# Optimization experiments

Hardware: AMD Instinct MI355X
Metric: run time of the kernel (lower is better)

Reference implementation:

```python
import jax, jax.numpy as jnp
import numpy as np
import math

D = 768; H = 12; DH = 64; LAT = 512; B = 2; L = 1024


def _rms(x, w, eps=1e-6):
    return w * x * jax.lax.rsqrt(jnp.mean(x * x, axis=-1, keepdims=True) + eps)


def _rope_tables(seq_len, dh):
    inv = 1.0 / (10000.0 ** (np.arange(0, dh, 2, dtype=np.float32) / dh))
    t = np.arange(seq_len, dtype=np.float32)
    f = np.outer(t, inv)
    emb = np.concatenate([f, f], axis=-1)
    return jnp.asarray(np.cos(emb))[None, :, None, :], jnp.asarray(np.sin(emb))[None, :, None, :]


def _rope(x, cos, sin):
    x1, x2 = jnp.split(x, 2, axis=-1)
    return x * cos + jnp.concatenate([-x2, x1], axis=-1) * sin


def setup_inputs():
    key = jax.random.key(0)
    ks = jax.random.split(key, 8)
    s = 0.02
    return {
        'x': jax.random.normal(ks[0], (B, L, D), jnp.float32),
        'w_ln': jnp.ones((D,), jnp.float32),
        'w_compress': jax.random.normal(ks[1], (D, LAT), jnp.float32) * s,
        'w_qkv': jax.random.normal(ks[2], (LAT, 3 * D), jnp.float32) * s,
        'w_reso': jax.random.normal(ks[3], (LAT, H * 4), jnp.float32) * s,
        'w_qn': jnp.ones((DH,), jnp.float32),
        'w_kn': jnp.ones((DH,), jnp.float32),
        'head_decay': jnp.linspace(-3.0, 1.0, H).astype(jnp.float32),
        'temperature': jnp.ones((1,), jnp.float32) * 0.5,
        'w_out_gate': jax.random.normal(ks[4], (LAT, D), jnp.float32) * s,
        'w_proj': jax.random.normal(ks[5], (D, D), jnp.float32) * s,
        'w_memnorm': jnp.ones((D,), jnp.float32),
    }


def reference(x, w_ln, w_compress, w_qkv, w_reso, w_qn, w_kn, head_decay, temperature, w_out_gate, w_proj, w_memnorm):
    cos, sin = _rope_tables(L, DH)
    xn = _rms(x, w_ln)
    latent = jax.nn.silu(xn @ w_compress)                        # (B,L,LAT)
    q, k, v = jnp.split(latent @ w_qkv, 3, axis=-1)
    q = _rope(_rms(q.reshape(B, L, H, DH), w_qn), cos, sin)
    k = _rope(_rms(k.reshape(B, L, H, DH), w_kn), cos, sin)
    v_f = v.reshape(B, L, H, DH)
    q_f = jax.nn.elu(q) + 1.0
    k_f = jax.nn.elu(k) + 1.0
    params = (latent @ w_reso).reshape(B, L, H, 4)
    sem_amp, sem_phase, ctx_amp, ctx_phase = [params[..., i] for i in range(4)]
    sem_phase = jax.nn.sigmoid(sem_phase) * math.pi
    ctx_phase = jax.nn.sigmoid(ctx_phase) * math.pi
    decay = jnp.clip(0.3 + 0.65 * jax.nn.sigmoid(head_decay), 1e-5, 0.999)   # (H,)
    gate = jnp.clip(jax.nn.sigmoid(jax.nn.sigmoid(sem_amp) * jax.nn.sigmoid(ctx_amp)
                                   * jnp.cos(sem_phase - ctx_phase) * temperature[0]) * 1.2 - 0.1,
                    0.05, 0.95)                                  # (B,L,H)
    one_m = (1.0 - decay)[None, None, :]                          # (1,1,H)
    kv_in = jnp.einsum('blhd,blhe->blhde', k_f, v_f) * gate[..., None, None] * one_m[..., None, None]
    z_in = k_f * one_m[..., None]
    # cumulative log-decay -> df, same as torch cumsum of constant per-step log_decay
    cum_log = jnp.arange(1, L + 1, dtype=jnp.float32)[:, None] * jnp.log(decay)[None, :]
    df = jnp.exp(cum_log)[None, :, :, None]                       # (1,L,H,1)
    kv_states = jnp.cumsum(kv_in / (df[..., None] + 1e-8), axis=1) * df[..., None]
    z_states = jnp.cumsum(z_in / (df + 1e-8), axis=1) * df
    out_num = jnp.einsum('blhd,blhde->blhe', q_f, kv_states)
    den = jnp.clip(jnp.sum(q_f * z_states, axis=-1, keepdims=True), 1e-5, None)
    out = (out_num / den).reshape(B, L, D)
    return (_rms(out, w_memnorm) @ w_proj) * jax.nn.silu(latent @ w_out_gate)
```

## Files before the change

kernel.cpp:

```cpp
#include <hip/hip_runtime.h>
#include <hip/hip_bf16.h>
#include <math.h>

#define D_MODEL 768
#define NHEAD   12
#define LATD    512
#define BATCH   2
#define SEQ     1024
#define NROWS   (BATCH*SEQ)
#define NCHUNK  (SEQ/64)
#define NBH     (BATCH*NHEAD)
#define NFUSE   3200
#define PQ      72

using short8 = __attribute__((ext_vector_type(8))) short;
using f32x4  = __attribute__((ext_vector_type(4))) float;

__device__ __forceinline__ float sigf(float x){ return 1.f/(1.f+expf(-x)); }
__device__ __forceinline__ float decay_of(float hd){
  float d = 0.3f + 0.65f*sigf(hd);
  return fminf(fmaxf(d, 1e-5f), 0.999f);
}
__device__ __forceinline__ unsigned short f2b(float f){
  __hip_bfloat16 h = __float2bfloat16(f);
  return *reinterpret_cast<unsigned short*>(&h);
}
__device__ __forceinline__ float bf2f(unsigned short u){
  unsigned int x = ((unsigned int)u) << 16;
  return __uint_as_float(x);
}
__device__ __forceinline__ void async16(const unsigned short* g, unsigned short* l){
  __builtin_amdgcn_global_load_lds((const __attribute__((address_space(1))) void*)g,
                                   (__attribute__((address_space(3))) void*)l, 16, 0, 0);
}

__device__ __forceinline__ void rms_row(const float* __restrict__ xr,
    const float* __restrict__ w, unsigned short* __restrict__ yr,
    int tid, float* red)
{
  float v0 = xr[tid], v1 = xr[tid+256], v2 = xr[tid+512];
  float s = v0*v0 + v1*v1 + v2*v2;
  #pragma unroll
  for (int off=32; off; off>>=1) s += __shfl_xor(s, off, 64);
  if ((tid & 63) == 0) red[tid>>6] = s;
  __syncthreads();
  s = red[0]+red[1]+red[2]+red[3];
  float sc = rsqrtf(s*(1.f/(float)D_MODEL) + 1e-6f);
  yr[tid]     = f2b(v0*sc*w[tid]);
  yr[tid+256] = f2b(v1*sc*w[tid+256]);
  yr[tid+512] = f2b(v2*sc*w[tid+512]);
}

__global__ __launch_bounds__(256) void k_rmsnorm_bf(const float* __restrict__ x,
    const float* __restrict__ w, unsigned short* __restrict__ y)
{
  __shared__ float red[4];
  int row = blockIdx.x, tid = threadIdx.x;
  rms_row(x + (size_t)row*D_MODEL, w, y + (size_t)row*D_MODEL, tid, red);
}

__global__ __launch_bounds__(256) void k_prep(
    const float* __restrict__ x, const float* __restrict__ w_ln,
    unsigned short* __restrict__ xn,
    const float* __restrict__ wc, const float* __restrict__ wq,
    const float* __restrict__ wr, const float* __restrict__ wg,
    const float* __restrict__ wp,
    unsigned short* __restrict__ wtc, unsigned short* __restrict__ wtq,
    unsigned short* __restrict__ wtg, unsigned short* __restrict__ wtp)
{
  __shared__ unsigned short tile[64][65];
  __shared__ float red[4];
  int blk = blockIdx.x, t = threadIdx.x;
  if (blk >= 640){
    int row = blk - 640;
    rms_row(x + (size_t)row*D_MODEL, w_ln, xn + (size_t)row*D_MODEL, t, red);
    return;
  }
  const float* W; unsigned short* WT; int K, N, bx, by;
  if (blk < 96){ W=wc; WT=wtc; K=768; N=512; bx=blk&7; by=blk>>3; }
  else if (blk < 384){ int i=blk-96;  W=wq; WT=wtq; K=512; N=2304; bx=i%36; by=i/36; }
  else if (blk < 480){ int i=blk-384; W=wg; WT=wtg; K=512; N=768;  bx=i%12; by=i/12; }
  else if (blk < 624){ int i=blk-480; W=wp; WT=wtp; K=768; N=768;  bx=i%12; by=i/12; }
  else {
    int i = blk - 624;
    #pragma unroll
    for (int j=0;j<16;j++){
      int e = i*4096 + t + j*256;
      int n = 2304 + (e >> 9), k = e & 511;
      float v = (n < 2352) ? wr[(size_t)k*48 + (n-2304)] : 0.f;
      wtq[(size_t)n*512 + k] = f2b(v);
    }
    return;
  }
  int k0 = by*64, n0 = bx*64, cr = t >> 6, cc = t & 63;
  #pragma unroll
  for (int i=0;i<16;i++){
    int r = cr + i*4;
    tile[r][cc] = f2b(W[(size_t)(k0+r)*N + n0 + cc]);
  }
  __syncthreads();
  #pragma unroll
  for (int i=0;i<16;i++){
    int nn = cr + i*4;
    WT[(size_t)(n0+nn)*K + k0 + cc] = tile[cc][nn];
  }
}

__global__ __launch_bounds__(256) void k_gemm64(const unsigned short* __restrict__ A,
    const unsigned short* __restrict__ BT, float* __restrict__ Cf,
    unsigned short* __restrict__ Cb, const unsigned short* __restrict__ auxb,
    int M, int N, int K, int act)
{
  __shared__ unsigned short As[64*64];
  __shared__ unsigned short Bs[64*64];
  int tid = threadIdx.x;
  int w = tid >> 6, lane = tid & 63;
  int m16 = lane & 15, quad = lane >> 4;
  int bm = blockIdx.y*64, bn = blockIdx.x*64;

  f32x4 acc[4];
  #pragma unroll
  for (int nt=0;nt<4;nt++) acc[nt] = (f32x4){0.f,0.f,0.f,0.f};

  for (int kk = 0; kk < K; kk += 64){
    #pragma unroll
    for (int i=0;i<2;i++){
      int g = (w*2 + i)*64 + lane;
      int m = g >> 3, c = (g & 7) ^ (m & 7);
      async16(A  + (size_t)(bm+m)*K + kk + c*8, As + (w*2+i)*512);
      async16(BT + (size_t)(bn+m)*K + kk + c*8, Bs + (w*2+i)*512);
    }
    __syncthreads();
    #pragma unroll
    for (int s=0;s<2;s++){
      int row = w*16 + m16;
      short8 af = *(const short8*)(As + (row*8 + ((s*4 + quad) ^ (row & 7)))*8);
      #pragma unroll
      for (int nt=0;nt<4;nt++){
        int n = nt*16 + m16;
        short8 bf = *(const short8*)(Bs + (n*8 + ((s*4 + quad) ^ (n & 7)))*8);
        acc[nt] = __builtin_amdgcn_mfma_f32_16x16x32_bf16(af, bf, acc[nt], 0, 0, 0);
      }
    }
    __syncthreads();
  }
  #pragma unroll
  for (int r=0;r<4;r++){
    int row = bm + w*16 + quad*4 + r;
    #pragma unroll
    for (int nt=0;nt<4;nt++){
      int col = bn + nt*16 + m16;
      float v = acc[nt][r];
      if (act == 1) v = v/(1.f + __expf(-v));
      else if (act == 2) v *= bf2f(auxb[(size_t)row*N + col]);
      if (Cf) Cf[(size_t)row*N + col] = v;
      if (Cb) Cb[(size_t)row*N + col] = f2b(v);
    }
  }
}

__global__ __launch_bounds__(256) void k_gemm_fused(const unsigned short* __restrict__ A,
    const unsigned short* __restrict__ BT, const float* __restrict__ w_qn,
    const float* __restrict__ w_kn, const float* __restrict__ hdec,
    const float* __restrict__ temp, unsigned short* __restrict__ qf,
    unsigned short* __restrict__ kf, unsigned short* __restrict__ vf,
    float* __restrict__ cKV, float* __restrict__ cG,
    unsigned short* __restrict__ gateb)
{
  __shared__ __align__(16) unsigned short SM[2*128*64];
  unsigned short* As = SM;
  unsigned short* Bs = SM + 128*64;
  const int K = LATD;
  int tid = threadIdx.x;
  int w = tid >> 6, lane = tid & 63;
  int wm = (w >> 1)*64, wn = (w & 1)*64;
  int m16 = lane & 15, quad = lane >> 4;
  int bm = blockIdx.y*128, bn = blockIdx.x*128;

  f32x4 acc[4][4];
  #pragma unroll
  for (int i=0;i<4;i++)
    #pragma unroll
    for (int j=0;j<4;j++) acc[i][j] = (f32x4){0.f,0.f,0.f,0.f};

  for (int kk = 0; kk < K; kk += 64){
    #pragma unroll
    for (int i=0;i<4;i++){
      int g = (w*4 + i)*64 + lane;
      int m = g >> 3, c = (g & 7) ^ (m & 7);
      async16(A  + (size_t)(bm+m)*K + kk + c*8, As + (w*4+i)*512);
      async16(BT + (size_t)(bn+m)*K + kk + c*8, Bs + (w*4+i)*512);
    }
    __syncthreads();
    #pragma unroll
    for (int s=0;s<2;s++){
      short8 af[4], bf[4];
      #pragma unroll
      for (int mt=0;mt<4;mt++){
        int m = wm + mt*16 + m16;
        int idx = m*8 + ((s*4 + quad) ^ (m & 7));
        af[mt] = *(const short8*)(As + idx*8);
      }
      #pragma unroll
      for (int nt=0;nt<4;nt++){
        int n = wn + nt*16 + m16;
        int idx = n*8 + ((s*4 + quad) ^ (n & 7));
        bf[nt] = *(const short8*)(Bs + idx*8);
      }
      #pragma unroll
      for (int mt=0;mt<4;mt++)
        #pragma unroll
        for (int nt=0;nt<4;nt++)
          acc[mt][nt] = __builtin_amdgcn_mfma_f32_16x16x32_bf16(af[mt], bf[nt], acc[mt][nt], 0, 0, 0);
    }
    __syncthreads();
  }

  int colbase = bn + wn;
  if (colbase < 2304){
    int sec = colbase >= 1536 ? 2 : (colbase >= 768 ? 1 : 0);
    int h = (colbase - sec*768) >> 6;
    if (sec == 2){
      #pragma unroll
      for (int mt=0;mt<4;mt++)
        #pragma unroll
        for (int r=0;r<4;r++){
          int row = bm + wm + mt*16 + quad*4 + r;
          int b = row >> 10, t = row & 1023;
          size_t ob = (((size_t)(b*NHEAD+h))*SEQ + t)*64;
          #pragma unroll
          for (int nt=0;nt<4;nt++)
            vf[ob + nt*16 + m16] = f2b(acc[mt][nt][r]);
        }
    } else {
      const float* wnp = sec ? w_kn : w_qn;
      unsigned short* of = sec ? kf : qf;
      float wv4[4];
      #pragma unroll
      for (int nt=0;nt<4;nt++) wv4[nt] = wnp[nt*16 + m16];
      float inv0 = exp2f(-(float)m16*(1.f/32.f)*13.28771237954945f);
      float inv1 = inv0 * 0.01f;
      #pragma unroll
      for (int mt=0;mt<4;mt++)
        #pragma unroll
        for (int r=0;r<4;r++){
          int row = bm + wm + mt*16 + quad*4 + r;
          int b = row >> 10, t = row & 1023;
          float s = 0.f;
          #pragma unroll
          for (int nt=0;nt<4;nt++) s += acc[mt][nt][r]*acc[mt][nt][r];
          s += __shfl_xor(s, 1, 64); s += __shfl_xor(s, 2, 64);
          s += __shfl_xor(s, 4, 64); s += __shfl_xor(s, 8, 64);
          float rs = rsqrtf(s*(1.f/64.f) + 1e-6f);
          float qv[4];
          #pragma unroll
          for (int nt=0;nt<4;nt++) qv[nt] = acc[mt][nt][r]*rs*wv4[nt];
          float s0,c0,s1,c1;
          __sincosf((float)t*inv0, &s0, &c0);
          __sincosf((float)t*inv1, &s1, &c1);
          size_t ob = (((size_t)(b*NHEAD+h))*SEQ + t)*64;
          #pragma unroll
          for (int nt=0;nt<4;nt++){
            float rot = (nt < 2) ? -qv[nt+2] : qv[nt-2];
            float cs = (nt & 1) ? c1 : c0, sn = (nt & 1) ? s1 : s0;
            float val = qv[nt]*cs + rot*sn;
            val = (val > 0.f) ? val + 1.f : __expf(val);
            of[ob + nt*16 + m16] = f2b(val);
          }
        }
    }
  } else if (colbase < 2432){
    float* pf = (float*)SM;
    if (colbase == 2304){
      #pragma unroll
      for (int mt=0;mt<4;mt++)
        #pragma unroll
        for (int r=0;r<4;r++){
          int rowl = wm + mt*16 + quad*4 + r;
          #pragma unroll
          for (int nt=0;nt<4;nt++){
            int p = nt*16 + m16;
            if (p < 48) pf[rowl*49 + p] = acc[mt][nt][r];
          }
        }
    }
    __syncthreads();
    float tv = temp[0];
    #pragma unroll
    for (int i=0;i<6;i++){
      int idx2 = tid + i*256;
      int rowl = idx2 / 12, h = idx2 - rowl*12;
      int row = bm + rowl, b = row >> 10, t = row & 1023;
      const float* pr = pf + rowl*49 + h*4;
      float sa = sigf(pr[0]);
      float sp = sigf(pr[1])*3.14159265358979323846f;
      float ca = sigf(pr[2]);
      float cp = sigf(pr[3])*3.14159265358979323846f;
      float z = sa*ca*cosf(sp - cp)*tv;
      float gate = fminf(fmaxf(sigf(z)*1.2f - 0.1f, 0.05f), 0.95f);
      float dd = decay_of(hdec[h]);
      float df = expf((float)(t+1)*logf(dd));
      float g = df/(df + 1e-8f);
      int ci = (b*NHEAD + h)*SEQ + t;
      cKV[ci] = g*gate*(1.f - dd);
      cG[ci]  = 1.f/gate;
    }
  } else {
    #pragma unroll
    for (int mt=0;mt<4;mt++)
      #pragma unroll
      for (int r=0;r<4;r++){
        int row = bm + wm + mt*16 + quad*4 + r;
        #pragma unroll
        for (int nt=0;nt<4;nt++){
          int gc = colbase + nt*16 + m16 - 2432;
          float v = acc[mt][nt][r];
          v = v/(1.f + __expf(-v));
          gateb[(size_t)row*D_MODEL + gc] = f2b(v);
        }
      }
  }
}

__global__ __launch_bounds__(256) void k_intra(const unsigned short* __restrict__ qf,
    const unsigned short* __restrict__ kf, const unsigned short* __restrict__ vf,
    const float* __restrict__ cKVb, const float* __restrict__ cGb,
    const float* __restrict__ hdec, float* __restrict__ numb,
    float* __restrict__ denb, float* __restrict__ Pb, float* __restrict__ zPb)
{
  __shared__ __align__(16) unsigned short Qb[64*PQ];
  __shared__ __align__(16) unsigned short Kb[64*PQ];
  __shared__ __align__(16) unsigned short KtS[64*PQ];
  __shared__ __align__(16) unsigned short Wb[64*PQ];
  __shared__ __align__(16) unsigned short Vt[80*PQ];
  __shared__ float cn[64], cps[64];
  int bid = blockIdx.x;
  int chunk = bid & 15, bh = bid >> 4, h = bh % NHEAD;
  int tid = threadIdx.x, w = tid >> 6, lane = tid & 63;
  int m16 = lane & 15, quad = lane >> 4;
  size_t base = ((size_t)bh*SEQ + chunk*64)*64;
  float d = decay_of(hdec[h]);
  float l2d = log2f(d);

  if (tid < 64){
    float c = cKVb[bh*SEQ + chunk*64 + tid];
    float pw = exp2f((float)(63 - tid)*l2d);
    cn[tid] = c;
    cps[tid] = c*pw;
    Vt[64*PQ + tid] = f2b(cGb[bh*SEQ + chunk*64 + tid]);
  }
  for (int i = tid; i < 15*PQ; i += 256) Vt[65*PQ + i] = 0;
  __syncthreads();

  #pragma unroll
  for (int i=0;i<2;i++){
    int g = tid + i*256;
    int r = g >> 3, c8 = (g & 7)*8;
    *(short8*)(Qb + r*PQ + c8) = *(const short8*)(qf + base + r*64 + c8);
    *(short8*)(Kb + r*PQ + c8) = *(const short8*)(kf + base + r*64 + c8);
  }
  {
    int s = tid & 63;
    float cpss = cps[s];
    #pragma unroll
    for (int i=0;i<2;i++){
      int c8 = ((tid >> 6) + i*4)*8;
      short8 vv = *(const short8*)(vf + base + s*64 + c8);
      short8 kk = *(const short8*)(kf + base + s*64 + c8);
      #pragma unroll
      for (int j=0;j<8;j++){
        Vt[(c8+j)*PQ + s] = ((unsigned short*)&vv)[j];
        KtS[(c8+j)*PQ + s] = f2b(bf2f(((unsigned short*)&kk)[j])*cpss);
      }
    }
  }
  __syncthreads();

  int trow = w*16 + quad*4;
  for (int stile=0; stile<4; stile++){
    if (stile > w){
      #pragma unroll
      for (int r=0;r<4;r++) Wb[(trow+r)*PQ + stile*16 + m16] = 0;
      continue;
    }
    f32x4 acc = (f32x4){0.f,0.f,0.f,0.f};
    #pragma unroll
    for (int ks=0;ks<2;ks++){
      short8 a = *(const short8*)(Qb + (w*16 + m16)*PQ + ks*32 + quad*8);
      short8 b = *(const short8*)(Kb + (stile*16 + m16)*PQ + ks*32 + quad*8);
      acc = __builtin_amdgcn_mfma_f32_16x16x32_bf16(a, b, acc, 0, 0, 0);
    }
    int s = stile*16 + m16;
    float cns = cn[s];
    #pragma unroll
    for (int r=0;r<4;r++){
      int t = trow + r;
      float wv = 0.f;
      if (s <= t) wv = acc[r]*exp2f((float)(t-s)*l2d)*cns;
      Wb[t*PQ + s] = f2b(wv);
    }
  }
  __syncthreads();

  {
    f32x4 acc[5];
    #pragma unroll
    for (int et=0;et<5;et++) acc[et] = (f32x4){0.f,0.f,0.f,0.f};
    #pragma unroll
    for (int et=0;et<5;et++)
      #pragma unroll
      for (int ks=0;ks<2;ks++){
        short8 a = *(const short8*)(Wb + (w*16 + m16)*PQ + ks*32 + quad*8);
        short8 b = *(const short8*)(Vt + (et*16 + m16)*PQ + ks*32 + quad*8);
        acc[et] = __builtin_amdgcn_mfma_f32_16x16x32_bf16(a, b, acc[et], 0, 0, 0);
      }
    #pragma unroll
    for (int et=0;et<4;et++)
      #pragma unroll
      for (int r=0;r<4;r++)
        numb[base + (size_t)(trow+r)*64 + et*16 + m16] = acc[et][r];
    if (m16 == 0){
      #pragma unroll
      for (int r=0;r<4;r++)
        denb[bh*SEQ + chunk*64 + trow + r] = acc[4][r];
    }
  }
  {
    #pragma unroll
    for (int j=0;j<5;j++){
      int tIdx = w + 4*j;
      int et = tIdx >> 2, dt = tIdx & 3;
      f32x4 acc = (f32x4){0.f,0.f,0.f,0.f};
      #pragma unroll
      for (int ks=0;ks<2;ks++){
        short8 a = *(const short8*)(Vt  + (et*16 + m16)*PQ + ks*32 + quad*8);
        short8 b = *(const short8*)(KtS + (dt*16 + m16)*PQ + ks*32 + quad*8);
        acc = __builtin_amdgcn_mfma_f32_16x16x32_bf16(a, b, acc, 0, 0, 0);
      }
      if (et < 4){
        #pragma unroll
        for (int r=0;r<4;r++)
          Pb[(size_t)bid*4096 + (et*16 + quad*4 + r)*64 + dt*16 + m16] = acc[r];
      } else {
        if (quad == 0) zPb[bid*64 + dt*16 + m16] = acc[0];
      }
    }
  }
}

__global__ __launch_bounds__(256) void k_scan(const float* __restrict__ Pb,
    const float* __restrict__ zPb, unsigned short* __restrict__ Sprev,
    unsigned short* __restrict__ zprev, const float* __restrict__ hdec)
{
  int bh = blockIdx.x >> 2, part = blockIdx.x & 3;
  int h = bh % NHEAD, tid = threadIdx.x;
  float d = decay_of(hdec[h]);
  float d64 = exp2f(64.f*log2f(d));
  int idx = part*1024 + tid*4;
  float4 S = make_float4(0.f,0.f,0.f,0.f);
  for (int c=0;c<NCHUNK;c++){
    size_t off = ((size_t)bh*NCHUNK + c)*4096 + idx;
    unsigned int lo = (unsigned int)f2b(S.x) | ((unsigned int)f2b(S.y) << 16);
    unsigned int hi = (unsigned int)f2b(S.z) | ((unsigned int)f2b(S.w) << 16);
    *(uint2*)(Sprev + off) = make_uint2(lo, hi);
    float4 p = *(const float4*)(Pb + off);
    S.x = S.x*d64 + p.x; S.y = S.y*d64 + p.y;
    S.z = S.z*d64 + p.z; S.w = S.w*d64 + p.w;
  }
  if (part == 0 && tid < 64){
    float z = 0.f;
    for (int c=0;c<NCHUNK;c++){
      int zoff = (bh*NCHUNK + c)*64 + tid;
      zprev[zoff] = f2b(z);
      z = z*d64 + zPb[zoff];
    }
  }
}

__global__ __launch_bounds__(256) void k_cross(const unsigned short* __restrict__ qf,
    const unsigned short* __restrict__ Sprev, const unsigned short* __restrict__ zprev,
    const float* __restrict__ numb, const float* __restrict__ denb,
    const float* __restrict__ hdec, float* __restrict__ attn)
{
  __shared__ __align__(16) unsigned short Qb[64*PQ];
  __shared__ __align__(16) unsigned short Sp[80*PQ];
  __shared__ float den_sm[64];
  int bid = blockIdx.x;
  int chunk = bid & 15, bh = bid >> 4, h = bh % NHEAD, b = bh / NHEAD;
  int tid = threadIdx.x, w = tid >> 6, lane = tid & 63;
  int m16 = lane & 15, quad = lane >> 4;
  size_t base = ((size_t)bh*SEQ + chunk*64)*64;
  float d = decay_of(hdec[h]);
  float l2d = log2f(d);

  #pragma unroll
  for (int i=0;i<2;i++){
    int g = tid + i*256;
    int r = g >> 3, c8 = (g & 7)*8;
    *(short8*)(Qb + r*PQ + c8) = *(const short8*)(qf + base + r*64 + c8);
    *(short8*)(Sp + r*PQ + c8) = *(const short8*)(Sprev + (size_t)bid*4096 + r*64 + c8);
  }
  if (tid < 64) Sp[64*PQ + tid] = zprev[bid*64 + tid];
  for (int i = tid; i < 15*PQ; i += 256) Sp[65*PQ + i] = 0;
  __syncthreads();

  f32x4 acc[5];
  #pragma unroll
  for (int et=0;et<5;et++) acc[et] = (f32x4){0.f,0.f,0.f,0.f};
  #pragma unroll
  for (int et=0;et<5;et++)
    #pragma unroll
    for (int ks=0;ks<2;ks++){
      short8 a = *(const short8*)(Qb + (w*16 + m16)*PQ + ks*32 + quad*8);
      short8 b = *(const short8*)(Sp + (et*16 + m16)*PQ + ks*32 + quad*8);
      acc[et] = __builtin_amdgcn_mfma_f32_16x16x32_bf16(a, b, acc[et], 0, 0, 0);
    }
  int trow = w*16 + quad*4;
  if (m16 == 0){
    #pragma unroll
    for (int r=0;r<4;r++){
      int tl = trow + r;
      float pw = exp2f((float)(tl+1)*l2d);
      float den = fmaxf(denb[bh*SEQ + chunk*64 + tl] + pw*acc[4][r], 1e-5f);
      den_sm[tl] = 1.f/den;
    }
  }
  __syncthreads();
  #pragma unroll
  for (int r=0;r<4;r++){
    int tl = trow + r;
    float pw = exp2f((float)(tl+1)*l2d);
    float invden = den_sm[tl];
    int tg = chunk*64 + tl;
    #pragma unroll
    for (int et=0;et<4;et++){
      int e = et*16 + m16;
      float nm = numb[base + (size_t)tl*64 + e] + pw*acc[et][r];
      attn[((size_t)(b*SEQ + tg))*D_MODEL + h*64 + e] = nm*invden;
    }
  }
}

extern "C" void kernel_launch(void* const* d_in, const int* in_sizes, int n_in,
                              void* d_out, int out_size, void* d_ws, size_t ws_size,
                              hipStream_t stream)
{
  (void)in_sizes; (void)n_in; (void)out_size; (void)ws_size;
  const float* x       = (const float*)d_in[0];
  const float* w_ln    = (const float*)d_in[1];
  const float* w_comp  = (const float*)d_in[2];
  const float* w_qkv   = (const float*)d_in[3];
  const float* w_reso  = (const float*)d_in[4];
  const float* w_qn    = (const float*)d_in[5];
  const float* w_kn    = (const float*)d_in[6];
  const float* hdec    = (const float*)d_in[7];
  const float* temp    = (const float*)d_in[8];
  const float* w_ogate = (const float*)d_in[9];
  const float* w_proj  = (const float*)d_in[10];
  const float* w_mn    = (const float*)d_in[11];
  float* ws = (float*)d_ws;
  float* out = (float*)d_out;

  const size_t o_cKV    = 0;
  const size_t o_cG     = o_cKV    + (size_t)NBH*SEQ;
  const size_t o_den    = o_cG     + (size_t)NBH*SEQ;
  const size_t o_P      = o_den    + (size_t)NBH*SEQ;
  const size_t o_zP     = o_P      + (size_t)NBH*NCHUNK*4096;
  const size_t o_attn   = o_zP     + (size_t)NBH*NCHUNK*64;
  const size_t o_numb   = o_attn   + (size_t)NROWS*D_MODEL;
  const size_t o_end    = o_numb   + (size_t)NBH*SEQ*64;

  unsigned short* bws = (unsigned short*)(ws + o_end);
  const size_t u_xn     = 0;
  const size_t u_latent = u_xn     + (size_t)NROWS*D_MODEL;
  const size_t u_memn   = u_latent + (size_t)NROWS*LATD;
  const size_t u_q      = u_memn   + (size_t)NROWS*D_MODEL;
  const size_t u_k      = u_q      + (size_t)NBH*SEQ*64;
  const size_t u_v      = u_k      + (size_t)NBH*SEQ*64;
  const size_t u_gate   = u_v      + (size_t)NBH*SEQ*64;
  const size_t u_S      = u_gate   + (size_t)NROWS*D_MODEL;
  const size_t u_zprev  = u_S      + (size_t)NBH*NCHUNK*4096;
  const size_t u_wtc    = u_zprev  + (size_t)NBH*NCHUNK*64;
  const size_t u_wtq    = u_wtc    + (size_t)LATD*D_MODEL;
  const size_t u_wtg    = u_wtq    + (size_t)2432*LATD;
  const size_t u_wtp    = u_wtg    + (size_t)D_MODEL*LATD;

  k_prep<<<2688, 256, 0, stream>>>(x, w_ln, bws + u_xn,
      w_comp, w_qkv, w_reso, w_ogate, w_proj,
      bws + u_wtc, bws + u_wtq, bws + u_wtg, bws + u_wtp);
  k_gemm64<<<dim3(LATD/64, NROWS/64), 256, 0, stream>>>(bws + u_xn, bws + u_wtc,
      nullptr, bws + u_latent, nullptr, NROWS, LATD, D_MODEL, 1);
  k_gemm_fused<<<dim3(NFUSE/128, NROWS/128), 256, 0, stream>>>(bws + u_latent, bws + u_wtq,
      w_qn, w_kn, hdec, temp, bws + u_q, bws + u_k, bws + u_v,
      ws + o_cKV, ws + o_cG, bws + u_gate);
  k_intra<<<NBH*NCHUNK, 256, 0, stream>>>(bws + u_q, bws + u_k, bws + u_v,
      ws + o_cKV, ws + o_cG, hdec, ws + o_numb, ws + o_den, ws + o_P, ws + o_zP);
  k_scan<<<NBH*4, 256, 0, stream>>>(ws + o_P, ws + o_zP, bws + u_S, bws + u_zprev, hdec);
  k_cross<<<NBH*NCHUNK, 256, 0, stream>>>(bws + u_q, bws + u_S, bws + u_zprev,
      ws + o_numb, ws + o_den, hdec, ws + o_attn);
  k_rmsnorm_bf<<<NROWS, 256, 0, stream>>>(ws + o_attn, w_mn, bws + u_memn);
  k_gemm64<<<dim3(D_MODEL/64, NROWS/64), 256, 0, stream>>>(bws + u_memn, bws + u_wtp,
      out, nullptr, bws + u_gate, NROWS, D_MODEL, D_MODEL, 2);
}
```

Measured before the change: 156.5 us.

## Fold chunk-state scan into cross kernel and swizzle block order for XCD locality

Removes the separate sequential scan kernel. Each cross block now rebuilds its prefix state directly as a decay-weighted sum over all earlier chunk contributions, which drops one launch and the Sprev/zprev round-trip through memory. In exchange, work grows quadratically with chunk index and Pb is re-read many times. Separately, the GEMM and cross kernels switch to a 1D grid with a mod-8 block swizzle, meant to group neighbouring tiles on the same XCD for better L2 reuse.

```diff
diff --git a/kernel.cpp b/kernel.cpp
--- a/kernel.cpp
+++ b/kernel.cpp
@@ -109,14 +109,17 @@
 __global__ __launch_bounds__(256) void k_gemm64(const unsigned short* __restrict__ A,
     const unsigned short* __restrict__ BT, float* __restrict__ Cf,
     unsigned short* __restrict__ Cb, const unsigned short* __restrict__ auxb,
-    int M, int N, int K, int act)
+    int M, int N, int K, int act, int NX)
 {
   __shared__ unsigned short As[64*64];
   __shared__ unsigned short Bs[64*64];
   int tid = threadIdx.x;
   int w = tid >> 6, lane = tid & 63;
   int m16 = lane & 15, quad = lane >> 4;
-  int bm = blockIdx.y*64, bn = blockIdx.x*64;
+  int bid = blockIdx.x, cpx = gridDim.x >> 3;
+  int swz = (bid & 7)*cpx + (bid >> 3);
+  int bx = swz % NX, by = swz / NX;
+  int bm = by*64, bn = bx*64;
 
   f32x4 acc[4];
   #pragma unroll
@@ -175,7 +178,10 @@
   int w = tid >> 6, lane = tid & 63;
   int wm = (w >> 1)*64, wn = (w & 1)*64;
   int m16 = lane & 15, quad = lane >> 4;
-  int bm = blockIdx.y*128, bn = blockIdx.x*128;
+  int bid = blockIdx.x;
+  int swz = (bid & 7)*50 + (bid >> 3);
+  int bx = swz >> 4, by = swz & 15;
+  int bm = by*128, bn = bx*128;
 
   f32x4 acc[4][4];
   #pragma unroll
@@ -448,37 +454,8 @@
   }
 }
 
-__global__ __launch_bounds__(256) void k_scan(const float* __restrict__ Pb,
-    const float* __restrict__ zPb, unsigned short* __restrict__ Sprev,
-    unsigned short* __restrict__ zprev, const float* __restrict__ hdec)
-{
-  int bh = blockIdx.x >> 2, part = blockIdx.x & 3;
-  int h = bh % NHEAD, tid = threadIdx.x;
-  float d = decay_of(hdec[h]);
-  float d64 = exp2f(64.f*log2f(d));
-  int idx = part*1024 + tid*4;
-  float4 S = make_float4(0.f,0.f,0.f,0.f);
-  for (int c=0;c<NCHUNK;c++){
-    size_t off = ((size_t)bh*NCHUNK + c)*4096 + idx;
-    unsigned int lo = (unsigned int)f2b(S.x) | ((unsigned int)f2b(S.y) << 16);
-    unsigned int hi = (unsigned int)f2b(S.z) | ((unsigned int)f2b(S.w) << 16);
-    *(uint2*)(Sprev + off) = make_uint2(lo, hi);
-    float4 p = *(const float4*)(Pb + off);
-    S.x = S.x*d64 + p.x; S.y = S.y*d64 + p.y;
-    S.z = S.z*d64 + p.z; S.w = S.w*d64 + p.w;
-  }
-  if (part == 0 && tid < 64){
-    float z = 0.f;
-    for (int c=0;c<NCHUNK;c++){
-      int zoff = (bh*NCHUNK + c)*64 + tid;
-      zprev[zoff] = f2b(z);
-      z = z*d64 + zPb[zoff];
-    }
-  }
-}
-
 __global__ __launch_bounds__(256) void k_cross(const unsigned short* __restrict__ qf,
-    const unsigned short* __restrict__ Sprev, const unsigned short* __restrict__ zprev,
+    const float* __restrict__ Pb, const float* __restrict__ zPb,
     const float* __restrict__ numb, const float* __restrict__ denb,
     const float* __restrict__ hdec, float* __restrict__ attn)
 {
@@ -486,21 +463,52 @@
   __shared__ __align__(16) unsigned short Sp[80*PQ];
   __shared__ float den_sm[64];
   int bid = blockIdx.x;
-  int chunk = bid & 15, bh = bid >> 4, h = bh % NHEAD, b = bh / NHEAD;
+  int swz = (bid & 7)*48 + (bid >> 3);
+  int chunk = swz & 15, bh = swz >> 4;
+  int h = bh % NHEAD, b = bh / NHEAD;
   int tid = threadIdx.x, w = tid >> 6, lane = tid & 63;
   int m16 = lane & 15, quad = lane >> 4;
   size_t base = ((size_t)bh*SEQ + chunk*64)*64;
   float d = decay_of(hdec[h]);
   float l2d = log2f(d);
+  float d64l2 = 64.f*l2d;
 
   #pragma unroll
   for (int i=0;i<2;i++){
     int g = tid + i*256;
     int r = g >> 3, c8 = (g & 7)*8;
     *(short8*)(Qb + r*PQ + c8) = *(const short8*)(qf + base + r*64 + c8);
-    *(short8*)(Sp + r*PQ + c8) = *(const short8*)(Sprev + (size_t)bid*4096 + r*64 + c8);
-  }
-  if (tid < 64) Sp[64*PQ + tid] = zprev[bid*64 + tid];
+  }
+
+  {
+    int r = tid >> 3, c8 = (tid & 7)*8;
+    float a0[8], a1[8];
+    #pragma unroll
+    for (int j=0;j<8;j++){ a0[j]=0.f; a1[j]=0.f; }
+    for (int c=0;c<chunk;c++){
+      float wgt = exp2f((float)(chunk-1-c)*d64l2);
+      const float* ps = Pb + ((size_t)(bh*NCHUNK + c))*4096;
+      float4 p0 = *(const float4*)(ps + r*64 + c8);
+      float4 p1 = *(const float4*)(ps + r*64 + c8 + 4);
+      float4 p2 = *(const float4*)(ps + (r+32)*64 + c8);
+      float4 p3 = *(const float4*)(ps + (r+32)*64 + c8 + 4);
+      a0[0]+=wgt*p0.x; a0[1]+=wgt*p0.y; a0[2]+=wgt*p0.z; a0[3]+=wgt*p0.w;
+      a0[4]+=wgt*p1.x; a0[5]+=wgt*p1.y; a0[6]+=wgt*p1.z; a0[7]+=wgt*p1.w;
+      a1[0]+=wgt*p2.x; a1[1]+=wgt*p2.y; a1[2]+=wgt*p2.z; a1[3]+=wgt*p2.w;
+      a1[4]+=wgt*p3.x; a1[5]+=wgt*p3.y; a1[6]+=wgt*p3.z; a1[7]+=wgt*p3.w;
+    }
+    #pragma unroll
+    for (int j=0;j<8;j++){
+      Sp[r*PQ + c8 + j]      = f2b(a0[j]);
+      Sp[(r+32)*PQ + c8 + j] = f2b(a1[j]);
+    }
+  }
+  if (tid < 64){
+    float z = 0.f;
+    for (int c=0;c<chunk;c++)
+      z += exp2f((float)(chunk-1-c)*d64l2) * zPb[(bh*NCHUNK + c)*64 + tid];
+    Sp[64*PQ + tid] = f2b(z);
+  }
   for (int i = tid; i < 15*PQ; i += 256) Sp[65*PQ + i] = 0;
   __syncthreads();
 
@@ -512,8 +520,8 @@
     #pragma unroll
     for (int ks=0;ks<2;ks++){
       short8 a = *(const short8*)(Qb + (w*16 + m16)*PQ + ks*32 + quad*8);
-      short8 b = *(const short8*)(Sp + (et*16 + m16)*PQ + ks*32 + quad*8);
-      acc[et] = __builtin_amdgcn_mfma_f32_16x16x32_bf16(a, b, acc[et], 0, 0, 0);
+      short8 bb = *(const short8*)(Sp + (et*16 + m16)*PQ + ks*32 + quad*8);
+      acc[et] = __builtin_amdgcn_mfma_f32_16x16x32_bf16(a, bb, acc[et], 0, 0, 0);
     }
   int trow = w*16 + quad*4;
   if (m16 == 0){
@@ -578,9 +586,7 @@
   const size_t u_k      = u_q      + (size_t)NBH*SEQ*64;
   const size_t u_v      = u_k      + (size_t)NBH*SEQ*64;
   const size_t u_gate   = u_v      + (size_t)NBH*SEQ*64;
-  const size_t u_S      = u_gate   + (size_t)NROWS*D_MODEL;
-  const size_t u_zprev  = u_S      + (size_t)NBH*NCHUNK*4096;
-  const size_t u_wtc    = u_zprev  + (size_t)NBH*NCHUNK*64;
+  const size_t u_wtc    = u_gate   + (size_t)NROWS*D_MODEL;
   const size_t u_wtq    = u_wtc    + (size_t)LATD*D_MODEL;
   const size_t u_wtg    = u_wtq    + (size_t)2432*LATD;
   const size_t u_wtp    = u_wtg    + (size_t)D_MODEL*LATD;
@@ -588,17 +594,16 @@
   k_prep<<<2688, 256, 0, stream>>>(x, w_ln, bws + u_xn,
       w_comp, w_qkv, w_reso, w_ogate, w_proj,
       bws + u_wtc, bws + u_wtq, bws + u_wtg, bws + u_wtp);
-  k_gemm64<<<dim3(LATD/64, NROWS/64), 256, 0, stream>>>(bws + u_xn, bws + u_wtc,
-      nullptr, bws + u_latent, nullptr, NROWS, LATD, D_MODEL, 1);
-  k_gemm_fused<<<dim3(NFUSE/128, NROWS/128), 256, 0, stream>>>(bws + u_latent, bws + u_wtq,
+  k_gemm64<<<256, 256, 0, stream>>>(bws + u_xn, bws + u_wtc,
+      nullptr, bws + u_latent, nullptr, NROWS, LATD, D_MODEL, 1, LATD/64);
+  k_gemm_fused<<<400, 256, 0, stream>>>(bws + u_latent, bws + u_wtq,
       w_qn, w_kn, hdec, temp, bws + u_q, bws + u_k, bws + u_v,
       ws + o_cKV, ws + o_cG, bws + u_gate);
   k_intra<<<NBH*NCHUNK, 256, 0, stream>>>(bws + u_q, bws + u_k, bws + u_v,
       ws + o_cKV, ws + o_cG, hdec, ws + o_numb, ws + o_den, ws + o_P, ws + o_zP);
-  k_scan<<<NBH*4, 256, 0, stream>>>(ws + o_P, ws + o_zP, bws + u_S, bws + u_zprev, hdec);
-  k_cross<<<NBH*NCHUNK, 256, 0, stream>>>(bws + u_q, bws + u_S, bws + u_zprev,
+  k_cross<<<NBH*NCHUNK, 256, 0, stream>>>(bws + u_q, ws + o_P, ws + o_zP,
       ws + o_numb, ws + o_den, hdec, ws + o_attn);
   k_rmsnorm_bf<<<NROWS, 256, 0, stream>>>(ws + o_attn, w_mn, bws + u_memn);
-  k_gemm64<<<dim3(D_MODEL/64, NROWS/64), 256, 0, stream>>>(bws + u_memn, bws + u_wtp,
-      out, nullptr, bws + u_gate, NROWS, D_MODEL, D_MODEL, 2);
-}
+  k_gemm64<<<384, 256, 0, stream>>>(bws + u_memn, bws + u_wtp,
+      out, nullptr, bws + u_gate, NROWS, D_MODEL, D_MODEL, 2, D_MODEL/64);
+}
```

After: 157.4 us. About the same (+0.6%).
